# Optimization experiments

Hardware: AMD Instinct MI355X
Metric: run time of the kernel (lower is better)

Reference implementation:

```python
import jax, jax.numpy as jnp
import numpy as np
import math

B, L, D = 8, 2048, 256
NUM_TYPES = 1
T_MAX = 200.0
SIGMA = 1.0


def setup_inputs() -> dict:
    key = jax.random.key(0)
    ks = jax.random.split(key, 12)
    event_type = jnp.ones((B, L), dtype=jnp.int64 if jax.config.jax_enable_x64 else jnp.int32)
    t = jax.random.uniform(ks[0], (B, L), dtype=jnp.float32) * T_MAX
    event_time = jnp.sort(t, axis=-1)
    s = 1.0 / math.sqrt(D)
    emb_weight = jax.random.normal(ks[1], (NUM_TYPES + 1, D), jnp.float32)
    emb_weight = emb_weight.at[0].set(0.0)  # padding_idx=0
    gate_w = jax.random.normal(ks[2], (2, D), jnp.float32) * s
    gate_b = jnp.zeros((2,), jnp.float32)
    ker_w = jax.random.normal(ks[3], (1, D), jnp.float32) * s
    ker_b = jnp.zeros((1,), jnp.float32)
    ln_gamma = jnp.ones((D,), jnp.float32)
    ln_beta = jnp.zeros((D,), jnp.float32)
    gen_input_w = jax.random.normal(ks[4], (D, D), jnp.float32) * s
    gen_noise_w = jax.random.normal(ks[5], (D, D), jnp.float32) * s
    gen_out_w = jax.random.normal(ks[6], (1, D), jnp.float32) * s
    gen_out_b = jnp.zeros((1,), jnp.float32)
    noise = jax.random.uniform(ks[7], (B, L, D), jnp.float32)  # torch.rand noise in Generator
    return dict(event_type=event_type, event_time=event_time, emb_weight=emb_weight,
                gate_w=gate_w, gate_b=gate_b, ker_w=ker_w, ker_b=ker_b,
                ln_gamma=ln_gamma, ln_beta=ln_beta, gen_input_w=gen_input_w,
                gen_noise_w=gen_noise_w, gen_out_w=gen_out_w, gen_out_b=gen_out_b,
                noise=noise)


def _softplus_beta(x, beta):
    return jax.nn.softplus(beta * x) / beta


def reference(event_type, event_time, emb_weight, gate_w, gate_b, ker_w, ker_b,
              ln_gamma, ln_beta, gen_input_w, gen_noise_w, gen_out_w, gen_out_b, noise):
    d_model = emb_weight.shape[-1]
    # ---- temporal positional encoding (this is `embedding`) ----
    pos_vec = jnp.power(10000.0, 2.0 * jnp.arange(d_model, dtype=jnp.float32) / d_model)
    t = event_time[:, :, None] / pos_vec                      # [B,L,D]
    idx = jnp.arange(d_model)
    temp_enc = jnp.where(idx % 2 == 0, jnp.sin(t), jnp.cos(t))
    # ---- type embedding ----
    te = emb_weight[event_type] * math.sqrt(d_model)          # [B,L,D]
    # ---- pairwise |t_i - t_j| ; xt[b,i,j]=t_i, xt_bar[b,i,j]=t_j ----
    dt = jnp.abs(event_time[:, :, None] - event_time[:, None, :])  # [B,L,L]
    # ---- squared exponential kernel: params depend only on row i (xd[b,i,j]=te[b,i]) ----
    ls = _softplus_beta(te @ ker_w.T + ker_b, 0.2)[..., 0]    # [B,L]
    scores_k = (SIGMA ** 2) * jnp.exp(-(dt ** 2) / (ls[:, :, None] ** 2))
    # ---- sigmoid gate ----
    p = jax.nn.sigmoid(te @ gate_w.T + gate_b)                # [B,L,2]
    l = p[..., 0][:, :, None]
    s = p[..., 1][:, :, None]
    gate = 1.0 + 0.5 * jnp.tanh((dt / T_MAX - l) / s)
    scores = scores_k * gate                                  # [B,L,L]
    # ---- causal mask: strictly-upper-triangle -> -1e10, then softmax ----
    causal = jnp.tril(jnp.ones((event_time.shape[1], event_time.shape[1]), jnp.bool_))
    scores = jnp.where(causal[None], scores, -1e10)
    attn = jax.nn.softmax(scores, axis=-1)
    # ---- hidden = attn @ temp_enc, layernorm ----
    hidden = jnp.einsum('bij,bjd->bid', attn, temp_enc)
    mu = hidden.mean(-1, keepdims=True)
    var = hidden.var(-1, keepdims=True)
    hidden = (hidden - mu) / jnp.sqrt(var + 1e-6) * ln_gamma + ln_beta
    # ---- Generator (dropout in eval = identity) ----
    h = jax.nn.relu(noise @ gen_noise_w.T + hidden @ gen_input_w.T)
    out = jax.nn.softplus(h @ gen_out_w.T + gen_out_b)[..., 0]  # [B,L]
    return out
```

## Files before the change

### kernel.cpp

```cpp
#include <hip/hip_runtime.h>
#include <hip/hip_bf16.h>

#define BD 8
#define LD 2048
#define DD 256

typedef unsigned short ushort_t;
typedef __attribute__((ext_vector_type(8))) short short8;
typedef __attribute__((ext_vector_type(4))) float floatx4;

__device__ __forceinline__ ushort_t f2bfu(float x) {
  __hip_bfloat16 h = __float2bfloat16(x);
  return *reinterpret_cast<ushort_t*>(&h);
}

__device__ __forceinline__ void dma16(const ushort_t* g, ushort_t* l) {
  __builtin_amdgcn_global_load_lds(
      (const __attribute__((address_space(1))) unsigned int*)g,
      (__attribute__((address_space(3))) unsigned int*)l,
      16, 0, 0);
}

__device__ __forceinline__ float sin_acc(float a) {
  float k = rintf(a * 0.15915494f);
  float r = __builtin_fmaf(-k, 6.2831855f, a);
  r = __builtin_fmaf(-k, -1.7484555e-7f, r);
  return __sinf(r);
}
__device__ __forceinline__ float cos_acc(float a) {
  float k = rintf(a * 0.15915494f);
  float r = __builtin_fmaf(-k, 6.2831855f, a);
  r = __builtin_fmaf(-k, -1.7484555e-7f, r);
  return __cosf(r);
}

__global__ __launch_bounds__(256) void k_dots(
    const float* __restrict__ embw, const float* __restrict__ gatew,
    const float* __restrict__ gateb, const float* __restrict__ kerw,
    const float* __restrict__ kerb, float* __restrict__ ptable)
{
  int d = threadIdx.x;
  int lane = d & 63, wvi = d >> 6;
  __shared__ float red[4][3];
  for (int ty = 0; ty < 2; ++ty) {
    float te = embw[ty * DD + d] * 16.0f;
    float p1 = te * kerw[d];
    float p2 = te * gatew[d];
    float p3 = te * gatew[DD + d];
    #pragma unroll
    for (int off = 32; off > 0; off >>= 1) {
      p1 += __shfl_xor(p1, off);
      p2 += __shfl_xor(p2, off);
      p3 += __shfl_xor(p3, off);
    }
    if (lane == 0) { red[wvi][0] = p1; red[wvi][1] = p2; red[wvi][2] = p3; }
    __syncthreads();
    if (d == 0) {
      float s1 = red[0][0] + red[1][0] + red[2][0] + red[3][0] + kerb[0];
      float s2 = red[0][1] + red[1][1] + red[2][1] + red[3][1] + gateb[0];
      float s3 = red[0][2] + red[1][2] + red[2][2] + red[3][2] + gateb[1];
      float z = 0.2f * s1;
      float sp = (z > 15.0f) ? z : log1pf(__expf(z));
      float ls = 5.0f * sp;
      ptable[ty * 4 + 0] = 1.0f / (ls * ls);
      ptable[ty * 4 + 1] = 1.0f / (1.0f + __expf(-s2));
      float s = 1.0f / (1.0f + __expf(-s3));
      ptable[ty * 4 + 2] = 1.0f / s;
    }
    __syncthreads();
  }
}

__global__ __launch_bounds__(256) void k_prep_enc(
    const float* __restrict__ etime, ushort_t* __restrict__ enc_bf)
{
  int bk = blockIdx.x;
  int tid = threadIdx.x;
  __shared__ float ts[32];
  if (tid < 32) ts[tid] = etime[(bk >> 6) * LD + (bk & 63) * 32 + tid];
  __syncthreads();
  uint4* dst = (uint4*)(enc_bf + (size_t)bk * 8192);
  const int jb = (tid & 3) * 8;
  #pragma unroll
  for (int jblk = 0; jblk < 4; ++jblk) {
    int d = jblk * 64 + (tid >> 2);
    float freq = __expf(-0.07195578416f * (float)d);
    unsigned int pk[4];
    #pragma unroll
    for (int p = 0; p < 4; ++p) {
      float a0 = ts[jb + 2 * p] * freq;
      float a1 = ts[jb + 2 * p + 1] * freq;
      float v0 = (d & 1) ? cos_acc(a0) : sin_acc(a0);
      float v1 = (d & 1) ? cos_acc(a1) : sin_acc(a1);
      pk[p] = (unsigned int)f2bfu(v0) | ((unsigned int)f2bfu(v1) << 16);
    }
    dst[jblk * 256 + tid] = make_uint4(pk[0], pk[1], pk[2], pk[3]);
  }
}

__global__ __launch_bounds__(256) void k_cast(
    const float* __restrict__ noise, const float* __restrict__ wn,
    const float* __restrict__ wi, ushort_t* __restrict__ noise_bf,
    ushort_t* __restrict__ wcat)
{
  int idx = blockIdx.x * 256 + threadIdx.x;
  if (idx < 1048576) {
    float4 f = ((const float4*)noise)[idx];
    ushort4 u;
    u.x = f2bfu(f.x); u.y = f2bfu(f.y); u.z = f2bfu(f.z); u.w = f2bfu(f.w);
    *(ushort4*)(noise_bf + (size_t)idx * 4) = u;
  } else {
    int p = idx - 1048576;
    int c = p >> 7;
    int k = (p & 127) * 4;
    const float* src = (k < 256) ? (wn + c * 256 + k) : (wi + c * 256 + (k - 256));
    float4 f = *(const float4*)src;
    ushort4 u;
    u.x = f2bfu(f.x); u.y = f2bfu(f.y); u.z = f2bfu(f.z); u.w = f2bfu(f.w);
    *(ushort4*)(wcat + (size_t)c * 512 + k) = u;
  }
}

__global__ __launch_bounds__(256, 4) void k_attn(
    const ushort_t* __restrict__ enc_bf, const float* __restrict__ etime,
    const int* __restrict__ etype, const float* __restrict__ ptable,
    const float* __restrict__ gamma, const float* __restrict__ beta,
    ushort_t* __restrict__ hidden_bf)
{
  __shared__ __align__(16) ushort_t stage[4][8192];
  const int tid = threadIdx.x;
  const int lane = tid & 63, wv = tid >> 6;
  const int bk = blockIdx.x;
  const int b = bk & 7;
  const int tl = 127 - (bk >> 3);
  const int base = b * LD;
  const int m = lane & 15, kg = lane >> 4;
  const int i = tl * 16 + m;
  const float ti = etime[base + i];
  const int ty = etype[base + i];
  const float il = ptable[ty * 4 + 0];
  const float ll = ptable[ty * 4 + 1];
  const float is2 = 2.0f * ptable[ty * 4 + 2];
  floatx4 acc[16];
  #pragma unroll
  for (int nt = 0; nt < 16; ++nt) acc[nt] = (floatx4){0.f, 0.f, 0.f, 0.f};
  const int nch = tl / 2 + 1;
  const ushort_t* __restrict__ encC = enc_bf + (size_t)(b * 64) * 8192;
  const int boff = m * 32 + kg * 8;
  ushort_t* mybuf = &stage[wv][0];
  for (int ch = wv; ch < nch; ch += 4) {
    const int j0 = ch * 32 + kg * 8;
    float4 tja = *(const float4*)(etime + base + j0);
    float4 tjb = *(const float4*)(etime + base + j0 + 4);
    __builtin_amdgcn_s_waitcnt(0xC07F);
    const ushort_t* gsrc = encC + (size_t)ch * 8192 + lane * 8;
    #pragma unroll
    for (int nt = 0; nt < 16; ++nt)
      dma16(gsrc + nt * 512, mybuf + nt * 512);
    float tj[8] = {tja.x, tja.y, tja.z, tja.w, tjb.x, tjb.y, tjb.z, tjb.w};
    short8 af;
    #pragma unroll
    for (int v = 0; v < 8; ++v) {
      float dt = fabsf(ti - tj[v]);
      float sk = __expf(-dt * dt * il);
      float rg = __builtin_amdgcn_rcpf(__expf((dt * 0.005f - ll) * is2) + 1.0f);
      float w = __expf(sk * (1.5f - rg));
      w = (j0 + v <= i) ? w : 0.0f;
      af[v] = (short)f2bfu(w);
    }
    __builtin_amdgcn_s_waitcnt(0x0F70);
    #pragma unroll
    for (int nt = 0; nt < 16; ++nt) {
      short8 bf = *(const short8*)(mybuf + nt * 512 + boff);
      acc[nt] = __builtin_amdgcn_mfma_f32_16x16x32_bf16(af, bf, acc[nt], 0, 0, 0);
    }
  }
  __syncthreads();
  floatx4* lds_acc = (floatx4*)&stage[0][0];
  if (wv != 0) {
    #pragma unroll
    for (int nt = 0; nt < 16; ++nt) lds_acc[(nt * 3 + (wv - 1)) * 64 + lane] = acc[nt];
  }
  __syncthreads();
  if (wv == 0) {
    #pragma unroll
    for (int nt = 0; nt < 16; ++nt) {
      acc[nt] += lds_acc[(nt * 3 + 0) * 64 + lane];
      acc[nt] += lds_acc[(nt * 3 + 1) * 64 + lane];
      acc[nt] += lds_acc[(nt * 3 + 2) * 64 + lane];
    }
    float gl[16], cl[16];
    #pragma unroll
    for (int nt = 0; nt < 16; ++nt) { gl[nt] = gamma[nt * 16 + m]; cl[nt] = beta[nt * 16 + m]; }
    const int q = lane >> 4;
    #pragma unroll
    for (int r = 0; r < 4; ++r) {
      float h[16];
      float sm = 0.0f, sq = 0.0f;
      #pragma unroll
      for (int nt = 0; nt < 16; ++nt) {
        h[nt] = acc[nt][r];
        sm += h[nt]; sq += h[nt] * h[nt];
      }
      #pragma unroll
      for (int off = 1; off < 16; off <<= 1) {
        sm += __shfl_xor(sm, off);
        sq += __shfl_xor(sq, off);
      }
      float mean = sm * (1.0f / 256.0f);
      float var = sq * (1.0f / 256.0f) - mean * mean;
      float rstd = rsqrtf(var + 1e-6f);
      const int row = q * 4 + r;
      ushort_t* dst = hidden_bf + ((size_t)(base + tl * 16 + row)) * DD + m;
      #pragma unroll
      for (int nt = 0; nt < 16; ++nt)
        dst[nt * 16] = f2bfu((h[nt] - mean) * rstd * gl[nt] + cl[nt]);
    }
  }
}

__global__ __launch_bounds__(256) void k_gen(
    const ushort_t* __restrict__ noise_bf, const ushort_t* __restrict__ hidden_bf,
    const ushort_t* __restrict__ wcat, const float* __restrict__ wout,
    const float* __restrict__ bout, float* __restrict__ out)
{
  __shared__ float pbuf[4][2][16];
  const int tid = threadIdx.x;
  const int lane = tid & 63, wv = tid >> 6;
  const int m = lane & 15, kg = lane >> 4;
  const int r0 = blockIdx.x * 32 + m;
  const ushort_t* __restrict__ an0 = noise_bf + (size_t)r0 * DD;
  const ushort_t* __restrict__ an1 = noise_bf + (size_t)(r0 + 16) * DD;
  const ushort_t* __restrict__ ah0 = hidden_bf + (size_t)r0 * DD;
  const ushort_t* __restrict__ ah1 = hidden_bf + (size_t)(r0 + 16) * DD;
  floatx4 acc[2][4];
  #pragma unroll
  for (int t = 0; t < 2; ++t)
    #pragma unroll
    for (int n = 0; n < 4; ++n) acc[t][n] = (floatx4){0.f, 0.f, 0.f, 0.f};
  const ushort_t* __restrict__ bbase = wcat + ((size_t)(wv * 4) * 16 + m) * 512 + kg * 8;
  #pragma unroll
  for (int ks = 0; ks < 16; ++ks) {
    const int koff = (ks & 7) * 32 + kg * 8;
    short8 a0 = *(const short8*)(((ks < 8) ? an0 : ah0) + koff);
    short8 a1 = *(const short8*)(((ks < 8) ? an1 : ah1) + koff);
    const ushort_t* bp = bbase + ks * 32;
    #pragma unroll
    for (int n = 0; n < 4; ++n) {
      short8 bf = *(const short8*)(bp + (size_t)n * 8192);
      acc[0][n] = __builtin_amdgcn_mfma_f32_16x16x32_bf16(a0, bf, acc[0][n], 0, 0, 0);
      acc[1][n] = __builtin_amdgcn_mfma_f32_16x16x32_bf16(a1, bf, acc[1][n], 0, 0, 0);
    }
  }
  float wo_l[4];
  #pragma unroll
  for (int n = 0; n < 4; ++n) wo_l[n] = wout[(wv * 4 + n) * 16 + m];
  #pragma unroll
  for (int t = 0; t < 2; ++t) {
    #pragma unroll
    for (int r4 = 0; r4 < 4; ++r4) {
      float p = 0.0f;
      #pragma unroll
      for (int n = 0; n < 4; ++n) p += fmaxf(acc[t][n][r4], 0.0f) * wo_l[n];
      #pragma unroll
      for (int off = 1; off < 16; off <<= 1) p += __shfl_xor(p, off);
      if (m == 0) pbuf[wv][t][kg * 4 + r4] = p;
    }
  }
  __syncthreads();
  if (tid < 32) {
    int t = tid >> 4, rr = tid & 15;
    float x = pbuf[0][t][rr] + pbuf[1][t][rr] + pbuf[2][t][rr] + pbuf[3][t][rr] + bout[0];
    float sp = (x > 15.0f) ? x : log1pf(__expf(x));
    out[blockIdx.x * 32 + t * 16 + rr] = sp;
  }
}

extern "C" void kernel_launch(void* const* d_in, const int* in_sizes, int n_in,
                              void* d_out, int out_size, void* d_ws, size_t ws_size,
                              hipStream_t stream) {
  const int*   etype = (const int*)d_in[0];
  const float* etime = (const float*)d_in[1];
  const float* embw  = (const float*)d_in[2];
  const float* gatew = (const float*)d_in[3];
  const float* gateb = (const float*)d_in[4];
  const float* kerw  = (const float*)d_in[5];
  const float* kerb  = (const float*)d_in[6];
  const float* gamma = (const float*)d_in[7];
  const float* beta  = (const float*)d_in[8];
  const float* wi    = (const float*)d_in[9];
  const float* wn    = (const float*)d_in[10];
  const float* wo    = (const float*)d_in[11];
  const float* bo    = (const float*)d_in[12];
  const float* noise = (const float*)d_in[13];
  float* out = (float*)d_out;

  char* w8 = (char*)d_ws;
  float* ptable       = (float*)(w8);
  ushort_t* enc_bf    = (ushort_t*)(w8 + 262144);
  ushort_t* hidden_bf = (ushort_t*)(w8 + 262144 + 8388608);
  ushort_t* noise_bf  = (ushort_t*)(w8 + 262144 + 2 * 8388608);
  ushort_t* wcat      = (ushort_t*)(w8 + 262144 + 3 * 8388608);

  k_dots<<<1, 256, 0, stream>>>(embw, gatew, gateb, kerw, kerb, ptable);
  k_prep_enc<<<512, 256, 0, stream>>>(etime, enc_bf);
  k_cast<<<4224, 256, 0, stream>>>(noise, wn, wi, noise_bf, wcat);
  k_attn<<<1024, 256, 0, stream>>>(enc_bf, etime, etype, ptable,
                                   gamma, beta, hidden_bf);
  k_gen<<<512, 256, 0, stream>>>(noise_bf, hidden_bf, wcat, wo, bo, out);
}
```

Measured before the change: 162.6 us.

## Merge prep kernels, double attention rows per block, fuse noise cast into generator

The three setup kernels are merged into a single launch, and the noise fp32-to-bf16 pass is dropped: the generator now converts noise in registers as it loads it. The attention kernel handles 32 query rows per block, so each staged encoding chunk feeds two MFMA accumulators, and the grid is halved. Gate and kernel constants are pre-scaled by log2(e) so exp2 can be used, and the causal mask is applied only on the diagonal chunk. The costs are higher register pressure (launch bounds lowered to 2 blocks), an extra cross-wave reduction round, and a fused generator that reads fp32 noise directly.

After: 148.9 us. -8.4%, faster.

```diff
diff --git a/kernel.cpp b/kernel.cpp
--- a/kernel.cpp
+++ b/kernel.cpp
@@ -4,6 +4,7 @@
 #define BD 8
 #define LD 2048
 #define DD 256
+#define LOG2E 1.4426950408889634f
 
 typedef unsigned short ushort_t;
 typedef __attribute__((ext_vector_type(8))) short short8;
@@ -12,6 +13,14 @@
 __device__ __forceinline__ ushort_t f2bfu(float x) {
   __hip_bfloat16 h = __float2bfloat16(x);
   return *reinterpret_cast<ushort_t*>(&h);
+}
+
+__device__ __forceinline__ float exp2fast(float x) {
+#if __has_builtin(__builtin_amdgcn_exp2f)
+  return __builtin_amdgcn_exp2f(x);
+#else
+  return __expf(x * 0.6931471805599453f);
+#endif
 }
 
 __device__ __forceinline__ void dma16(const ushort_t* g, ushort_t* l) {
@@ -34,83 +43,49 @@
   return __cosf(r);
 }
 
-__global__ __launch_bounds__(256) void k_dots(
-    const float* __restrict__ embw, const float* __restrict__ gatew,
-    const float* __restrict__ gateb, const float* __restrict__ kerw,
-    const float* __restrict__ kerb, float* __restrict__ ptable)
+__device__ __forceinline__ short8 pk8(float4 a, float4 b) {
+  short8 r;
+  r[0] = (short)f2bfu(a.x); r[1] = (short)f2bfu(a.y);
+  r[2] = (short)f2bfu(a.z); r[3] = (short)f2bfu(a.w);
+  r[4] = (short)f2bfu(b.x); r[5] = (short)f2bfu(b.y);
+  r[6] = (short)f2bfu(b.z); r[7] = (short)f2bfu(b.w);
+  return r;
+}
+
+__global__ __launch_bounds__(256) void k_prep(
+    const float* __restrict__ etime, const float* __restrict__ embw,
+    const float* __restrict__ gatew, const float* __restrict__ gateb,
+    const float* __restrict__ kerw, const float* __restrict__ kerb,
+    const float* __restrict__ wn, const float* __restrict__ wi,
+    ushort_t* __restrict__ enc_bf, ushort_t* __restrict__ wcat,
+    float* __restrict__ ptable)
 {
-  int d = threadIdx.x;
-  int lane = d & 63, wvi = d >> 6;
+  const int bk = blockIdx.x;
+  const int tid = threadIdx.x;
+  __shared__ float ts[32];
   __shared__ float red[4][3];
-  for (int ty = 0; ty < 2; ++ty) {
-    float te = embw[ty * DD + d] * 16.0f;
-    float p1 = te * kerw[d];
-    float p2 = te * gatew[d];
-    float p3 = te * gatew[DD + d];
-    #pragma unroll
-    for (int off = 32; off > 0; off >>= 1) {
-      p1 += __shfl_xor(p1, off);
-      p2 += __shfl_xor(p2, off);
-      p3 += __shfl_xor(p3, off);
-    }
-    if (lane == 0) { red[wvi][0] = p1; red[wvi][1] = p2; red[wvi][2] = p3; }
+  if (bk < 512) {
+    if (tid < 32) ts[tid] = etime[(bk >> 6) * LD + (bk & 63) * 32 + tid];
     __syncthreads();
-    if (d == 0) {
-      float s1 = red[0][0] + red[1][0] + red[2][0] + red[3][0] + kerb[0];
-      float s2 = red[0][1] + red[1][1] + red[2][1] + red[3][1] + gateb[0];
-      float s3 = red[0][2] + red[1][2] + red[2][2] + red[3][2] + gateb[1];
-      float z = 0.2f * s1;
-      float sp = (z > 15.0f) ? z : log1pf(__expf(z));
-      float ls = 5.0f * sp;
-      ptable[ty * 4 + 0] = 1.0f / (ls * ls);
-      ptable[ty * 4 + 1] = 1.0f / (1.0f + __expf(-s2));
-      float s = 1.0f / (1.0f + __expf(-s3));
-      ptable[ty * 4 + 2] = 1.0f / s;
-    }
-    __syncthreads();
-  }
-}
-
-__global__ __launch_bounds__(256) void k_prep_enc(
-    const float* __restrict__ etime, ushort_t* __restrict__ enc_bf)
-{
-  int bk = blockIdx.x;
-  int tid = threadIdx.x;
-  __shared__ float ts[32];
-  if (tid < 32) ts[tid] = etime[(bk >> 6) * LD + (bk & 63) * 32 + tid];
-  __syncthreads();
-  uint4* dst = (uint4*)(enc_bf + (size_t)bk * 8192);
-  const int jb = (tid & 3) * 8;
-  #pragma unroll
-  for (int jblk = 0; jblk < 4; ++jblk) {
-    int d = jblk * 64 + (tid >> 2);
-    float freq = __expf(-0.07195578416f * (float)d);
-    unsigned int pk[4];
-    #pragma unroll
-    for (int p = 0; p < 4; ++p) {
-      float a0 = ts[jb + 2 * p] * freq;
-      float a1 = ts[jb + 2 * p + 1] * freq;
-      float v0 = (d & 1) ? cos_acc(a0) : sin_acc(a0);
-      float v1 = (d & 1) ? cos_acc(a1) : sin_acc(a1);
-      pk[p] = (unsigned int)f2bfu(v0) | ((unsigned int)f2bfu(v1) << 16);
-    }
-    dst[jblk * 256 + tid] = make_uint4(pk[0], pk[1], pk[2], pk[3]);
-  }
-}
-
-__global__ __launch_bounds__(256) void k_cast(
-    const float* __restrict__ noise, const float* __restrict__ wn,
-    const float* __restrict__ wi, ushort_t* __restrict__ noise_bf,
-    ushort_t* __restrict__ wcat)
-{
-  int idx = blockIdx.x * 256 + threadIdx.x;
-  if (idx < 1048576) {
-    float4 f = ((const float4*)noise)[idx];
-    ushort4 u;
-    u.x = f2bfu(f.x); u.y = f2bfu(f.y); u.z = f2bfu(f.z); u.w = f2bfu(f.w);
-    *(ushort4*)(noise_bf + (size_t)idx * 4) = u;
-  } else {
-    int p = idx - 1048576;
+    uint4* dst = (uint4*)(enc_bf + (size_t)bk * 8192);
+    const int jb = (tid & 3) * 8;
+    #pragma unroll
+    for (int jblk = 0; jblk < 4; ++jblk) {
+      int d = jblk * 64 + (tid >> 2);
+      float freq = __expf(-0.07195578416f * (float)d);
+      unsigned int pk[4];
+      #pragma unroll
+      for (int p = 0; p < 4; ++p) {
+        float a0 = ts[jb + 2 * p] * freq;
+        float a1 = ts[jb + 2 * p + 1] * freq;
+        float v0 = (d & 1) ? cos_acc(a0) : sin_acc(a0);
+        float v1 = (d & 1) ? cos_acc(a1) : sin_acc(a1);
+        pk[p] = (unsigned int)f2bfu(v0) | ((unsigned int)f2bfu(v1) << 16);
+      }
+      dst[jblk * 256 + tid] = make_uint4(pk[0], pk[1], pk[2], pk[3]);
+    }
+  } else if (bk < 640) {
+    int p = (bk - 512) * 256 + tid;
     int c = p >> 7;
     int k = (p & 127) * 4;
     const float* src = (k < 256) ? (wn + c * 256 + k) : (wi + c * 256 + (k - 256));
@@ -118,10 +93,43 @@
     ushort4 u;
     u.x = f2bfu(f.x); u.y = f2bfu(f.y); u.z = f2bfu(f.z); u.w = f2bfu(f.w);
     *(ushort4*)(wcat + (size_t)c * 512 + k) = u;
-  }
-}
-
-__global__ __launch_bounds__(256, 4) void k_attn(
+  } else {
+    int d = tid;
+    int lane = d & 63, wvi = d >> 6;
+    for (int ty = 0; ty < 2; ++ty) {
+      float te = embw[ty * DD + d] * 16.0f;
+      float p1 = te * kerw[d];
+      float p2 = te * gatew[d];
+      float p3 = te * gatew[DD + d];
+      #pragma unroll
+      for (int off = 32; off > 0; off >>= 1) {
+        p1 += __shfl_xor(p1, off);
+        p2 += __shfl_xor(p2, off);
+        p3 += __shfl_xor(p3, off);
+      }
+      if (lane == 0) { red[wvi][0] = p1; red[wvi][1] = p2; red[wvi][2] = p3; }
+      __syncthreads();
+      if (d == 0) {
+        float s1 = red[0][0] + red[1][0] + red[2][0] + red[3][0] + kerb[0];
+        float s2 = red[0][1] + red[1][1] + red[2][1] + red[3][1] + gateb[0];
+        float s3 = red[0][2] + red[1][2] + red[2][2] + red[3][2] + gateb[1];
+        float z = 0.2f * s1;
+        float sp = (z > 15.0f) ? z : log1pf(__expf(z));
+        float ls = 5.0f * sp;
+        float il = 1.0f / (ls * ls);
+        float l  = 1.0f / (1.0f + __expf(-s2));
+        float s  = 1.0f / (1.0f + __expf(-s3));
+        float is2 = 2.0f / s;
+        ptable[ty * 4 + 0] = -il * LOG2E;
+        ptable[ty * 4 + 1] = 0.005f * is2 * LOG2E;
+        ptable[ty * 4 + 2] = l * is2 * LOG2E;
+      }
+      __syncthreads();
+    }
+  }
+}
+
+__global__ __launch_bounds__(256, 2) void k_attn(
     const ushort_t* __restrict__ enc_bf, const float* __restrict__ etime,
     const int* __restrict__ etype, const float* __restrict__ ptable,
     const float* __restrict__ gamma, const float* __restrict__ beta,
@@ -132,22 +140,49 @@
   const int lane = tid & 63, wv = tid >> 6;
   const int bk = blockIdx.x;
   const int b = bk & 7;
-  const int tl = 127 - (bk >> 3);
+  const int t64 = bk >> 3;
+  const int g = (bk < 256) ? (63 - t64) : (t64 - 32);
   const int base = b * LD;
   const int m = lane & 15, kg = lane >> 4;
-  const int i = tl * 16 + m;
-  const float ti = etime[base + i];
-  const int ty = etype[base + i];
-  const float il = ptable[ty * 4 + 0];
-  const float ll = ptable[ty * 4 + 1];
-  const float is2 = 2.0f * ptable[ty * 4 + 2];
-  floatx4 acc[16];
-  #pragma unroll
-  for (int nt = 0; nt < 16; ++nt) acc[nt] = (floatx4){0.f, 0.f, 0.f, 0.f};
-  const int nch = tl / 2 + 1;
+  const int i0 = g * 32 + m;
+  const int i1 = i0 + 16;
+  const float ti0 = etime[base + i0];
+  const float ti1 = etime[base + i1];
+  const int ty0 = etype[base + i0] * 4;
+  const int ty1 = etype[base + i1] * 4;
+  const float p00 = ptable[ty0 + 0], p01 = ptable[ty0 + 1], p02 = ptable[ty0 + 2];
+  const float p10 = ptable[ty1 + 0], p11 = ptable[ty1 + 1], p12 = ptable[ty1 + 2];
+  floatx4 acc0[16], acc1[16];
+  #pragma unroll
+  for (int nt = 0; nt < 16; ++nt) {
+    acc0[nt] = (floatx4){0.f, 0.f, 0.f, 0.f};
+    acc1[nt] = (floatx4){0.f, 0.f, 0.f, 0.f};
+  }
+  const int nch = g + 1;
   const ushort_t* __restrict__ encC = enc_bf + (size_t)(b * 64) * 8192;
   const int boff = m * 32 + kg * 8;
   ushort_t* mybuf = &stage[wv][0];
+
+#define WPAIR(V, MASKED)                                                      \
+  {                                                                           \
+    float d0 = ti0 - tj[V];                                                   \
+    float d1 = ti1 - tj[V];                                                   \
+    float e10 = exp2fast(d0 * d0 * p00);                                      \
+    float e11 = exp2fast(d1 * d1 * p10);                                      \
+    float z0 = __builtin_fmaf(fabsf(d0), p01, -p02);                          \
+    float z1 = __builtin_fmaf(fabsf(d1), p11, -p12);                          \
+    float r0 = __builtin_amdgcn_rcpf(exp2fast(z0) + 1.0f);                    \
+    float r1 = __builtin_amdgcn_rcpf(exp2fast(z1) + 1.0f);                    \
+    float w0 = exp2fast(e10 * __builtin_fmaf(r0, -LOG2E, 1.5f * LOG2E));      \
+    float w1 = exp2fast(e11 * __builtin_fmaf(r1, -LOG2E, 1.5f * LOG2E));      \
+    if (MASKED) {                                                             \
+      w0 = (j0 + V <= i0) ? w0 : 0.0f;                                        \
+      w1 = (j0 + V <= i1) ? w1 : 0.0f;                                        \
+    }                                                                         \
+    af0[V] = (short)f2bfu(w0);                                                \
+    af1[V] = (short)f2bfu(w1);                                                \
+  }
+
   for (int ch = wv; ch < nch; ch += 4) {
     const int j0 = ch * 32 + kg * 8;
     float4 tja = *(const float4*)(etime + base + j0);
@@ -158,48 +193,65 @@
     for (int nt = 0; nt < 16; ++nt)
       dma16(gsrc + nt * 512, mybuf + nt * 512);
     float tj[8] = {tja.x, tja.y, tja.z, tja.w, tjb.x, tjb.y, tjb.z, tjb.w};
-    short8 af;
-    #pragma unroll
-    for (int v = 0; v < 8; ++v) {
-      float dt = fabsf(ti - tj[v]);
-      float sk = __expf(-dt * dt * il);
-      float rg = __builtin_amdgcn_rcpf(__expf((dt * 0.005f - ll) * is2) + 1.0f);
-      float w = __expf(sk * (1.5f - rg));
-      w = (j0 + v <= i) ? w : 0.0f;
-      af[v] = (short)f2bfu(w);
+    short8 af0, af1;
+    if (ch < g) {
+      #pragma unroll
+      for (int v = 0; v < 8; ++v) WPAIR(v, false)
+    } else {
+      #pragma unroll
+      for (int v = 0; v < 8; ++v) WPAIR(v, true)
     }
     __builtin_amdgcn_s_waitcnt(0x0F70);
     #pragma unroll
     for (int nt = 0; nt < 16; ++nt) {
       short8 bf = *(const short8*)(mybuf + nt * 512 + boff);
-      acc[nt] = __builtin_amdgcn_mfma_f32_16x16x32_bf16(af, bf, acc[nt], 0, 0, 0);
-    }
-  }
-  __syncthreads();
-  floatx4* lds_acc = (floatx4*)&stage[0][0];
+      acc0[nt] = __builtin_amdgcn_mfma_f32_16x16x32_bf16(af0, bf, acc0[nt], 0, 0, 0);
+      acc1[nt] = __builtin_amdgcn_mfma_f32_16x16x32_bf16(af1, bf, acc1[nt], 0, 0, 0);
+    }
+  }
+#undef WPAIR
+
+  __syncthreads();
+  floatx4* lacc = (floatx4*)&stage[0][0];
   if (wv != 0) {
     #pragma unroll
-    for (int nt = 0; nt < 16; ++nt) lds_acc[(nt * 3 + (wv - 1)) * 64 + lane] = acc[nt];
+    for (int nt = 0; nt < 16; ++nt) lacc[((wv - 1) * 16 + nt) * 64 + lane] = acc0[nt];
   }
   __syncthreads();
   if (wv == 0) {
     #pragma unroll
-    for (int nt = 0; nt < 16; ++nt) {
-      acc[nt] += lds_acc[(nt * 3 + 0) * 64 + lane];
-      acc[nt] += lds_acc[(nt * 3 + 1) * 64 + lane];
-      acc[nt] += lds_acc[(nt * 3 + 2) * 64 + lane];
-    }
+    for (int nt = 0; nt < 16; ++nt)
+      acc0[nt] = acc0[nt] + lacc[nt * 64 + lane]
+                          + lacc[(16 + nt) * 64 + lane]
+                          + lacc[(32 + nt) * 64 + lane];
+  }
+  __syncthreads();
+  if (wv != 1) {
+    const int widx = (wv == 0) ? 0 : (wv - 1);
+    #pragma unroll
+    for (int nt = 0; nt < 16; ++nt) lacc[(widx * 16 + nt) * 64 + lane] = acc1[nt];
+  }
+  __syncthreads();
+  if (wv == 1) {
+    #pragma unroll
+    for (int nt = 0; nt < 16; ++nt)
+      acc0[nt] = acc1[nt] + lacc[nt * 64 + lane]
+                          + lacc[(16 + nt) * 64 + lane]
+                          + lacc[(32 + nt) * 64 + lane];
+  }
+  if (wv < 2) {
     float gl[16], cl[16];
     #pragma unroll
     for (int nt = 0; nt < 16; ++nt) { gl[nt] = gamma[nt * 16 + m]; cl[nt] = beta[nt * 16 + m]; }
     const int q = lane >> 4;
+    const int row0 = base + g * 32 + wv * 16;
     #pragma unroll
     for (int r = 0; r < 4; ++r) {
       float h[16];
       float sm = 0.0f, sq = 0.0f;
       #pragma unroll
       for (int nt = 0; nt < 16; ++nt) {
-        h[nt] = acc[nt][r];
+        h[nt] = acc0[nt][r];
         sm += h[nt]; sq += h[nt] * h[nt];
       }
       #pragma unroll
@@ -210,8 +262,7 @@
       float mean = sm * (1.0f / 256.0f);
       float var = sq * (1.0f / 256.0f) - mean * mean;
       float rstd = rsqrtf(var + 1e-6f);
-      const int row = q * 4 + r;
-      ushort_t* dst = hidden_bf + ((size_t)(base + tl * 16 + row)) * DD + m;
+      ushort_t* dst = hidden_bf + ((size_t)(row0 + q * 4 + r)) * DD + m;
       #pragma unroll
       for (int nt = 0; nt < 16; ++nt)
         dst[nt * 16] = f2bfu((h[nt] - mean) * rstd * gl[nt] + cl[nt]);
@@ -220,7 +271,7 @@
 }
 
 __global__ __launch_bounds__(256) void k_gen(
-    const ushort_t* __restrict__ noise_bf, const ushort_t* __restrict__ hidden_bf,
+    const float* __restrict__ noise, const ushort_t* __restrict__ hidden_bf,
     const ushort_t* __restrict__ wcat, const float* __restrict__ wout,
     const float* __restrict__ bout, float* __restrict__ out)
 {
@@ -229,8 +280,8 @@
   const int lane = tid & 63, wv = tid >> 6;
   const int m = lane & 15, kg = lane >> 4;
   const int r0 = blockIdx.x * 32 + m;
-  const ushort_t* __restrict__ an0 = noise_bf + (size_t)r0 * DD;
-  const ushort_t* __restrict__ an1 = noise_bf + (size_t)(r0 + 16) * DD;
+  const float* __restrict__ nf0 = noise + (size_t)r0 * DD;
+  const float* __restrict__ nf1 = noise + (size_t)(r0 + 16) * DD;
   const ushort_t* __restrict__ ah0 = hidden_bf + (size_t)r0 * DD;
   const ushort_t* __restrict__ ah1 = hidden_bf + (size_t)(r0 + 16) * DD;
   floatx4 acc[2][4];
@@ -242,8 +293,18 @@
   #pragma unroll
   for (int ks = 0; ks < 16; ++ks) {
     const int koff = (ks & 7) * 32 + kg * 8;
-    short8 a0 = *(const short8*)(((ks < 8) ? an0 : ah0) + koff);
-    short8 a1 = *(const short8*)(((ks < 8) ? an1 : ah1) + koff);
+    short8 a0, a1;
+    if (ks < 8) {
+      float4 fa = *(const float4*)(nf0 + koff);
+      float4 fb = *(const float4*)(nf0 + koff + 4);
+      a0 = pk8(fa, fb);
+      fa = *(const float4*)(nf1 + koff);
+      fb = *(const float4*)(nf1 + koff + 4);
+      a1 = pk8(fa, fb);
+    } else {
+      a0 = *(const short8*)(ah0 + koff);
+      a1 = *(const short8*)(ah1 + koff);
+    }
     const ushort_t* bp = bbase + ks * 32;
     #pragma unroll
     for (int n = 0; n < 4; ++n) {
@@ -299,13 +360,11 @@
   float* ptable       = (float*)(w8);
   ushort_t* enc_bf    = (ushort_t*)(w8 + 262144);
   ushort_t* hidden_bf = (ushort_t*)(w8 + 262144 + 8388608);
-  ushort_t* noise_bf  = (ushort_t*)(w8 + 262144 + 2 * 8388608);
-  ushort_t* wcat      = (ushort_t*)(w8 + 262144 + 3 * 8388608);
-
-  k_dots<<<1, 256, 0, stream>>>(embw, gatew, gateb, kerw, kerb, ptable);
-  k_prep_enc<<<512, 256, 0, stream>>>(etime, enc_bf);
-  k_cast<<<4224, 256, 0, stream>>>(noise, wn, wi, noise_bf, wcat);
-  k_attn<<<1024, 256, 0, stream>>>(enc_bf, etime, etype, ptable,
-                                   gamma, beta, hidden_bf);
-  k_gen<<<512, 256, 0, stream>>>(noise_bf, hidden_bf, wcat, wo, bo, out);
-}
+  ushort_t* wcat      = (ushort_t*)(w8 + 262144 + 2 * 8388608);
+
+  k_prep<<<641, 256, 0, stream>>>(etime, embw, gatew, gateb, kerw, kerb,
+                                  wn, wi, enc_bf, wcat, ptable);
+  k_attn<<<512, 256, 0, stream>>>(enc_bf, etime, etype, ptable,
+                                  gamma, beta, hidden_bf);
+  k_gen<<<512, 256, 0, stream>>>(noise, hidden_bf, wcat, wo, bo, out);
+}
```
